# Optimization experiments

Measured on AMD Instinct MI355X. Metric: run time of the kernel, lower is better.

Reference implementation:

```python
import jax, jax.numpy as jnp
import numpy as np

N_NODES = 100000
D_SRC = 128
D_DST = 128
D_OUT = 256
N_EDGES = 600000


def setup_inputs() -> dict:
    key = jax.random.key(0)
    k1, k2, k3, k4, k5 = jax.random.split(key, 5)
    x_src = jax.random.normal(k1, (N_NODES, D_SRC), dtype=jnp.float32)
    x_dst = jax.random.normal(k2, (N_NODES, D_DST), dtype=jnp.float32)
    edge_index = jax.random.randint(k3, (2, N_EDGES), 0, N_NODES, dtype=jnp.int64)
    # Linear(in_src + in_dst, out): torch stores W as [out, in]
    fan_in = D_SRC + D_DST
    bound = 1.0 / np.sqrt(fan_in)
    W = jax.random.uniform(k4, (D_OUT, fan_in), minval=-bound, maxval=bound, dtype=jnp.float32)
    b = jax.random.uniform(k5, (D_OUT,), minval=-bound, maxval=bound, dtype=jnp.float32)
    return {"x_src": x_src, "x_dst": x_dst, "edge_index": edge_index, "W": W, "b": b}


def reference(x_src, x_dst, edge_index, W, b):
    src_idx, dst_idx = edge_index[0], edge_index[1]
    n_dst = x_dst.shape[0]
    x_j = x_src[src_idx]                                  # [E, D_SRC] gather
    summed = jax.ops.segment_sum(x_j, dst_idx, num_segments=n_dst)   # [N, D_SRC]
    count = jax.ops.segment_sum(jnp.ones((src_idx.shape[0],), dtype=x_src.dtype),
                                dst_idx, num_segments=n_dst)          # [N]
    agg = summed / jnp.maximum(count, 1.0)[:, None]        # scatter-mean
    h = jnp.concatenate([x_dst, agg], axis=-1)             # [N, D_DST+D_SRC]
    return jax.nn.relu(h @ W.T + b)                        # [N, D_OUT]
```

## Files before the change

kernel.cpp:

```cpp
#include <hip/hip_runtime.h>

#define N_NODES 100000
#define D_SRC 128
#define D_OUT 256
#define K_DIM 256
#define CAP 32
#define OVF_CAP 2048

typedef __attribute__((ext_vector_type(8))) short short8;
typedef __attribute__((ext_vector_type(4))) float float4v;

__device__ inline unsigned short f2bf(float f) {
    unsigned int u = __float_as_uint(f);
    u += 0x7FFF + ((u >> 16) & 1);
    return (unsigned short)(u >> 16);
}
__device__ inline float bf_lo(unsigned int u) { return __uint_as_float(u << 16); }
__device__ inline float bf_hi(unsigned int u) { return __uint_as_float(u & 0xFFFF0000u); }

__global__ __launch_bounds__(256) void bucket_kernel(
    const int* __restrict__ ei,
    int* __restrict__ deg,
    int* __restrict__ ovf_cnt,
    int* __restrict__ ovf,
    int* __restrict__ bucket,
    int n_edges)
{
    int e = blockIdx.x * 256 + threadIdx.x;
    if (e >= n_edges) return;
    int s = ei[e];
    int d = ei[n_edges + e];
    int pos = atomicAdd(deg + d, 1);
    if (pos < CAP) {
        bucket[(size_t)d * CAP + pos] = s;
    } else {
        int o = atomicAdd(ovf_cnt, 1);
        if (o < OVF_CAP) { ovf[2 * o] = s; ovf[2 * o + 1] = d; }
    }
}

__global__ __launch_bounds__(256) void pack_src_kernel(
    const float* __restrict__ x, unsigned short* __restrict__ xb)
{
    int i = blockIdx.x * 256 + threadIdx.x;
    float4 v = ((const float4*)x)[i];
    ushort4 o;
    o.x = f2bf(v.x); o.y = f2bf(v.y); o.z = f2bf(v.z); o.w = f2bf(v.w);
    ((ushort4*)xb)[i] = o;
}

__global__ __launch_bounds__(256) void convert_w_kernel(
    const float* __restrict__ W, unsigned short* __restrict__ Wb)
{
    int i = blockIdx.x * 256 + threadIdx.x;
    float4 v = ((const float4*)W)[i];
    ushort4 o;
    o.x = f2bf(v.x); o.y = f2bf(v.y); o.z = f2bf(v.z); o.w = f2bf(v.w);
    ((ushort4*)Wb)[i] = o;
}

__global__ __launch_bounds__(256) void gather_kernel(
    const unsigned short* __restrict__ xsb,
    const int*   __restrict__ deg,
    const int*   __restrict__ bucket,
    const int*   __restrict__ ovf_cnt,
    const int*   __restrict__ ovf,
    unsigned short* __restrict__ aggb)
{
    int node = blockIdx.x * 4 + (threadIdx.x >> 6);
    if (node >= N_NODES) return;
    int lane = threadIdx.x & 63;

    int dtot = deg[node];
    int n = (dtot < CAP) ? dtot : CAP;

    int idx = bucket[(size_t)node * CAP + (lane & 31)];

    float ax = 0.f, ay = 0.f;
    int i = 0;
    for (; i + 4 <= n; i += 4) {
        int s0 = __shfl(idx, i);
        int s1 = __shfl(idx, i + 1);
        int s2 = __shfl(idx, i + 2);
        int s3 = __shfl(idx, i + 3);
        unsigned int u0 = ((const unsigned int*)(xsb + (size_t)s0 * D_SRC))[lane];
        unsigned int u1 = ((const unsigned int*)(xsb + (size_t)s1 * D_SRC))[lane];
        unsigned int u2 = ((const unsigned int*)(xsb + (size_t)s2 * D_SRC))[lane];
        unsigned int u3 = ((const unsigned int*)(xsb + (size_t)s3 * D_SRC))[lane];
        ax += bf_lo(u0) + bf_lo(u1) + bf_lo(u2) + bf_lo(u3);
        ay += bf_hi(u0) + bf_hi(u1) + bf_hi(u2) + bf_hi(u3);
    }
    for (; i < n; ++i) {
        int s0 = __shfl(idx, i);
        unsigned int u0 = ((const unsigned int*)(xsb + (size_t)s0 * D_SRC))[lane];
        ax += bf_lo(u0);
        ay += bf_hi(u0);
    }

    if (dtot > CAP) {
        int oc = *ovf_cnt;
        if (oc > OVF_CAP) oc = OVF_CAP;
        for (int o = 0; o < oc; ++o) {
            if (ovf[2 * o + 1] == node) {
                int s0 = ovf[2 * o];
                unsigned int u0 = ((const unsigned int*)(xsb + (size_t)s0 * D_SRC))[lane];
                ax += bf_lo(u0);
                ay += bf_hi(u0);
            }
        }
    }

    float inv = 1.0f / (float)((dtot > 1) ? dtot : 1);
    unsigned int packed = (unsigned int)f2bf(ax * inv)
                        | ((unsigned int)f2bf(ay * inv) << 16);
    ((unsigned int*)(aggb + (size_t)node * D_SRC))[lane] = packed;
}

__global__ __launch_bounds__(256) void mfma_gemm_kernel(
    const float* __restrict__ x_dst,
    const unsigned short* __restrict__ aggb,
    const unsigned short* __restrict__ Wb,
    const float* __restrict__ bias,
    float*       __restrict__ out)
{
    __shared__ float eps[4][16][68];

    int wave = threadIdx.x >> 6;
    int lane = threadIdx.x & 63;
    int lrow = lane & 15;
    int kq   = lane >> 4;
    int m0 = blockIdx.x * 64;
    int n0 = wave * 64;

    float4v acc[4][4];
    #pragma unroll
    for (int i = 0; i < 4; ++i)
        #pragma unroll
        for (int j = 0; j < 4; ++j)
            acc[i][j] = (float4v){0.f, 0.f, 0.f, 0.f};

    int  rowv[4];
    bool rok[4];
    #pragma unroll
    for (int mf = 0; mf < 4; ++mf) {
        rowv[mf] = m0 + mf * 16 + lrow;
        rok[mf]  = rowv[mf] < N_NODES;
    }

    const short8 zfrag = (short8){0,0,0,0,0,0,0,0};

    #pragma unroll
    for (int kc = 0; kc < 8; ++kc) {
        const int k0 = kc * 32;
        short8 afrag[4], bfrag[4];

        if (kc < 4) {
            #pragma unroll
            for (int mf = 0; mf < 4; ++mf) {
                float4 v0 = make_float4(0.f, 0.f, 0.f, 0.f);
                float4 v1 = v0;
                if (rok[mf]) {
                    const float* p = x_dst + (size_t)rowv[mf] * D_SRC + k0 + kq * 8;
                    v0 = *(const float4*)p;
                    v1 = *(const float4*)(p + 4);
                }
                union { unsigned short s[8]; short8 v; } pk;
                pk.s[0] = f2bf(v0.x); pk.s[1] = f2bf(v0.y);
                pk.s[2] = f2bf(v0.z); pk.s[3] = f2bf(v0.w);
                pk.s[4] = f2bf(v1.x); pk.s[5] = f2bf(v1.y);
                pk.s[6] = f2bf(v1.z); pk.s[7] = f2bf(v1.w);
                afrag[mf] = pk.v;
            }
        } else {
            #pragma unroll
            for (int mf = 0; mf < 4; ++mf)
                afrag[mf] = rok[mf]
                    ? *(const short8*)(aggb + (size_t)rowv[mf] * D_SRC + (k0 - 128) + kq * 8)
                    : zfrag;
        }

        #pragma unroll
        for (int nf = 0; nf < 4; ++nf)
            bfrag[nf] = *(const short8*)(Wb + (size_t)(n0 + nf * 16 + lrow) * K_DIM + k0 + kq * 8);

        #pragma unroll
        for (int mf = 0; mf < 4; ++mf)
            #pragma unroll
            for (int nf = 0; nf < 4; ++nf)
                acc[mf][nf] = __builtin_amdgcn_mfma_f32_16x16x32_bf16(
                    afrag[mf], bfrag[nf], acc[mf][nf], 0, 0, 0);
    }

    float bv[4];
    #pragma unroll
    for (int nf = 0; nf < 4; ++nf)
        bv[nf] = bias[n0 + nf * 16 + lrow];

    int srow   = lane >> 4;
    int schunk = lane & 15;

    #pragma unroll
    for (int mf = 0; mf < 4; ++mf) {
        #pragma unroll
        for (int nf = 0; nf < 4; ++nf)
            #pragma unroll
            for (int r = 0; r < 4; ++r)
                eps[wave][kq * 4 + r][nf * 16 + lrow] =
                    fmaxf(acc[mf][nf][r] + bv[nf], 0.f);
        __syncthreads();
        #pragma unroll
        for (int c = 0; c < 4; ++c) {
            int row  = c * 4 + srow;
            float4 v = *(const float4*)&eps[wave][row][schunk * 4];
            int grow = m0 + mf * 16 + row;
            if (grow < N_NODES)
                *(float4*)(out + (size_t)grow * D_OUT + n0 + schunk * 4) = v;
        }
        __syncthreads();
    }
}

extern "C" void kernel_launch(void* const* d_in, const int* in_sizes, int n_in,
                              void* d_out, int out_size, void* d_ws, size_t ws_size,
                              hipStream_t stream) {
    const float* x_src = (const float*)d_in[0];
    const float* x_dst = (const float*)d_in[1];
    const int*   ei    = (const int*)d_in[2];
    const float* W     = (const float*)d_in[3];
    const float* bias  = (const float*)d_in[4];
    float* out = (float*)d_out;

    int n_edges = in_sizes[2] / 2;

    int* deg     = (int*)d_ws;
    int* ovf_cnt = deg + N_NODES;
    int* ovf     = ovf_cnt + 4;
    int* bucket  = ovf + OVF_CAP * 2;
    unsigned short* aggb = (unsigned short*)(bucket + (size_t)N_NODES * CAP);
    unsigned short* Wb   = aggb + (size_t)N_NODES * D_SRC;
    unsigned short* xsb  = Wb + (size_t)D_OUT * K_DIM;

    hipMemsetAsync(d_ws, 0, (N_NODES + 4) * sizeof(int), stream);

    bucket_kernel<<<(n_edges + 255) / 256, 256, 0, stream>>>(
        ei, deg, ovf_cnt, ovf, bucket, n_edges);

    pack_src_kernel<<<(N_NODES * D_SRC / 4) / 256, 256, 0, stream>>>(x_src, xsb);

    convert_w_kernel<<<(D_OUT * K_DIM / 4) / 256, 256, 0, stream>>>(W, Wb);

    gather_kernel<<<(N_NODES + 3) / 4, 256, 0, stream>>>(
        xsb, deg, bucket, ovf_cnt, ovf, aggb);

    mfma_gemm_kernel<<<(N_NODES + 63) / 64, 256, 0, stream>>>(
        x_dst, aggb, Wb, bias, out);
}
```

Before: 331.4 us.

## Pre-swizzle GEMM operands into MFMA fragment layout and double-buffer fragment loads

Adds a pre-pass that converts x_dst to bf16 and stores it in the MFMA fragment order. W and the aggregated features are also written in that order, so each lane of the GEMM does one contiguous short8 load per fragment. The GEMM now prefetches the next k-chunk's fragments into a second register set, and the per-wave epilogue uses LDS waitcnts instead of block-wide barriers. The bucket and packed-source scratch buffers move into the output buffer to free workspace. The cost is an extra full read and write pass over x_dst and higher register pressure from the double buffers.

```diff
diff --git a/kernel.cpp b/kernel.cpp
--- a/kernel.cpp
+++ b/kernel.cpp
@@ -49,14 +49,38 @@
     ((ushort4*)xb)[i] = o;
 }
 
-__global__ __launch_bounds__(256) void convert_w_kernel(
-    const float* __restrict__ W, unsigned short* __restrict__ Wb)
-{
-    int i = blockIdx.x * 256 + threadIdx.x;
-    float4 v = ((const float4*)W)[i];
-    ushort4 o;
-    o.x = f2bf(v.x); o.y = f2bf(v.y); o.z = f2bf(v.z); o.w = f2bf(v.w);
-    ((ushort4*)Wb)[i] = o;
+__global__ __launch_bounds__(256) void pack_dst_sw_kernel(
+    const float* __restrict__ x, unsigned short* __restrict__ xdsw)
+{
+    int t = blockIdx.x * 256 + threadIdx.x;
+    int r = t >> 4;
+    int g = t & 15;
+    const float4* p = (const float4*)(x + (size_t)r * 128 + g * 8);
+    float4 v0 = p[0], v1 = p[1];
+    union { unsigned short s[8]; short8 v; } pk;
+    pk.s[0] = f2bf(v0.x); pk.s[1] = f2bf(v0.y);
+    pk.s[2] = f2bf(v0.z); pk.s[3] = f2bf(v0.w);
+    pk.s[4] = f2bf(v1.x); pk.s[5] = f2bf(v1.y);
+    pk.s[6] = f2bf(v1.z); pk.s[7] = f2bf(v1.w);
+    size_t gr = ((size_t)(r >> 4) * 4 + (g >> 2)) * 64 + (r & 15) + ((g & 3) << 4);
+    ((short8*)xdsw)[gr] = pk.v;
+}
+
+__global__ __launch_bounds__(256) void convert_w_sw_kernel(
+    const float* __restrict__ W, unsigned short* __restrict__ wsw)
+{
+    int t = blockIdx.x * 256 + threadIdx.x;
+    int r = t >> 5;
+    int g = t & 31;
+    const float4* p = (const float4*)(W + (size_t)r * 256 + g * 8);
+    float4 v0 = p[0], v1 = p[1];
+    union { unsigned short s[8]; short8 v; } pk;
+    pk.s[0] = f2bf(v0.x); pk.s[1] = f2bf(v0.y);
+    pk.s[2] = f2bf(v0.z); pk.s[3] = f2bf(v0.w);
+    pk.s[4] = f2bf(v1.x); pk.s[5] = f2bf(v1.y);
+    pk.s[6] = f2bf(v1.z); pk.s[7] = f2bf(v1.w);
+    size_t gr = ((size_t)(r >> 4) * 8 + (g >> 2)) * 64 + (r & 15) + ((g & 3) << 4);
+    ((short8*)wsw)[gr] = pk.v;
 }
 
 __global__ __launch_bounds__(256) void gather_kernel(
@@ -65,7 +89,7 @@
     const int*   __restrict__ bucket,
     const int*   __restrict__ ovf_cnt,
     const int*   __restrict__ ovf,
-    unsigned short* __restrict__ aggb)
+    unsigned int* __restrict__ aggsw)
 {
     int node = blockIdx.x * 4 + (threadIdx.x >> 6);
     if (node >= N_NODES) return;
@@ -113,13 +137,15 @@
     float inv = 1.0f / (float)((dtot > 1) ? dtot : 1);
     unsigned int packed = (unsigned int)f2bf(ax * inv)
                         | ((unsigned int)f2bf(ay * inv) << 16);
-    ((unsigned int*)(aggb + (size_t)node * D_SRC))[lane] = packed;
+    size_t dw = ((size_t)(node >> 4) * 4 + (lane >> 4)) * 256
+              + (size_t)((node & 15) + 16 * ((lane >> 2) & 3)) * 4 + (lane & 3);
+    aggsw[dw] = packed;
 }
 
 __global__ __launch_bounds__(256) void mfma_gemm_kernel(
-    const float* __restrict__ x_dst,
-    const unsigned short* __restrict__ aggb,
-    const unsigned short* __restrict__ Wb,
+    const short8* __restrict__ xdsw,
+    const short8* __restrict__ aggsw,
+    const short8* __restrict__ wsw,
     const float* __restrict__ bias,
     float*       __restrict__ out)
 {
@@ -129,8 +155,17 @@
     int lane = threadIdx.x & 63;
     int lrow = lane & 15;
     int kq   = lane >> 4;
-    int m0 = blockIdx.x * 64;
-    int n0 = wave * 64;
+    int mb   = blockIdx.x;
+    int m0   = mb * 64;
+    int n0   = wave * 64;
+
+    bool mok[4];
+    #pragma unroll
+    for (int mf = 0; mf < 4; ++mf) mok[mf] = (m0 + mf * 16) < N_NODES;
+
+    const short8* Ax = xdsw  + (size_t)mb * 1024 + lane;
+    const short8* Ag = aggsw + (size_t)mb * 1024 + lane;
+    const short8* Bw = wsw   + (size_t)wave * 2048 + lane;
 
     float4v acc[4][4];
     #pragma unroll
@@ -139,56 +174,36 @@
         for (int j = 0; j < 4; ++j)
             acc[i][j] = (float4v){0.f, 0.f, 0.f, 0.f};
 
-    int  rowv[4];
-    bool rok[4];
-    #pragma unroll
-    for (int mf = 0; mf < 4; ++mf) {
-        rowv[mf] = m0 + mf * 16 + lrow;
-        rok[mf]  = rowv[mf] < N_NODES;
-    }
-
     const short8 zfrag = (short8){0,0,0,0,0,0,0,0};
+    short8 a[2][4], b[2][4];
+
+    #pragma unroll
+    for (int mf = 0; mf < 4; ++mf)
+        a[0][mf] = mok[mf] ? Ax[mf * 256] : zfrag;
+    #pragma unroll
+    for (int nf = 0; nf < 4; ++nf)
+        b[0][nf] = Bw[nf * 512];
 
     #pragma unroll
     for (int kc = 0; kc < 8; ++kc) {
-        const int k0 = kc * 32;
-        short8 afrag[4], bfrag[4];
-
-        if (kc < 4) {
-            #pragma unroll
-            for (int mf = 0; mf < 4; ++mf) {
-                float4 v0 = make_float4(0.f, 0.f, 0.f, 0.f);
-                float4 v1 = v0;
-                if (rok[mf]) {
-                    const float* p = x_dst + (size_t)rowv[mf] * D_SRC + k0 + kq * 8;
-                    v0 = *(const float4*)p;
-                    v1 = *(const float4*)(p + 4);
-                }
-                union { unsigned short s[8]; short8 v; } pk;
-                pk.s[0] = f2bf(v0.x); pk.s[1] = f2bf(v0.y);
-                pk.s[2] = f2bf(v0.z); pk.s[3] = f2bf(v0.w);
-                pk.s[4] = f2bf(v1.x); pk.s[5] = f2bf(v1.y);
-                pk.s[6] = f2bf(v1.z); pk.s[7] = f2bf(v1.w);
-                afrag[mf] = pk.v;
-            }
-        } else {
+        const int cur = kc & 1, nxt = cur ^ 1;
+        if (kc < 7) {
+            const int k1 = kc + 1;
+            const short8* A = (k1 < 4) ? Ax : Ag;
+            const int kk = (k1 < 4) ? k1 : (k1 - 4);
             #pragma unroll
             for (int mf = 0; mf < 4; ++mf)
-                afrag[mf] = rok[mf]
-                    ? *(const short8*)(aggb + (size_t)rowv[mf] * D_SRC + (k0 - 128) + kq * 8)
-                    : zfrag;
+                a[nxt][mf] = mok[mf] ? A[mf * 256 + kk * 64] : zfrag;
+            #pragma unroll
+            for (int nf = 0; nf < 4; ++nf)
+                b[nxt][nf] = Bw[nf * 512 + k1 * 64];
         }
-
-        #pragma unroll
-        for (int nf = 0; nf < 4; ++nf)
-            bfrag[nf] = *(const short8*)(Wb + (size_t)(n0 + nf * 16 + lrow) * K_DIM + k0 + kq * 8);
-
         #pragma unroll
         for (int mf = 0; mf < 4; ++mf)
             #pragma unroll
             for (int nf = 0; nf < 4; ++nf)
                 acc[mf][nf] = __builtin_amdgcn_mfma_f32_16x16x32_bf16(
-                    afrag[mf], bfrag[nf], acc[mf][nf], 0, 0, 0);
+                    a[cur][mf], b[cur][nf], acc[mf][nf], 0, 0, 0);
     }
 
     float bv[4];
@@ -201,22 +216,22 @@
 
     #pragma unroll
     for (int mf = 0; mf < 4; ++mf) {
+        if (!mok[mf]) continue;
         #pragma unroll
         for (int nf = 0; nf < 4; ++nf)
             #pragma unroll
             for (int r = 0; r < 4; ++r)
                 eps[wave][kq * 4 + r][nf * 16 + lrow] =
                     fmaxf(acc[mf][nf][r] + bv[nf], 0.f);
-        __syncthreads();
+        asm volatile("s_waitcnt lgkmcnt(0)" ::: "memory");
         #pragma unroll
         for (int c = 0; c < 4; ++c) {
             int row  = c * 4 + srow;
             float4 v = *(const float4*)&eps[wave][row][schunk * 4];
             int grow = m0 + mf * 16 + row;
-            if (grow < N_NODES)
-                *(float4*)(out + (size_t)grow * D_OUT + n0 + schunk * 4) = v;
+            *(float4*)(out + (size_t)grow * D_OUT + n0 + schunk * 4) = v;
         }
-        __syncthreads();
+        asm volatile("s_waitcnt lgkmcnt(0)" ::: "memory");
     }
 }
 
@@ -235,10 +250,12 @@
     int* deg     = (int*)d_ws;
     int* ovf_cnt = deg + N_NODES;
     int* ovf     = ovf_cnt + 4;
-    int* bucket  = ovf + OVF_CAP * 2;
-    unsigned short* aggb = (unsigned short*)(bucket + (size_t)N_NODES * CAP);
-    unsigned short* Wb   = aggb + (size_t)N_NODES * D_SRC;
-    unsigned short* xsb  = Wb + (size_t)D_OUT * K_DIM;
+    unsigned short* wsw   = (unsigned short*)(ovf + OVF_CAP * 2);
+    unsigned short* aggsw = wsw + (size_t)D_OUT * K_DIM;
+    unsigned short* xdsw  = aggsw + (size_t)(N_NODES / 16) * 4 * 64 * 8;
+
+    int* bucket = (int*)d_out;
+    unsigned short* xsb = (unsigned short*)(bucket + (size_t)N_NODES * CAP);
 
     hipMemsetAsync(d_ws, 0, (N_NODES + 4) * sizeof(int), stream);
 
@@ -247,11 +264,13 @@
 
     pack_src_kernel<<<(N_NODES * D_SRC / 4) / 256, 256, 0, stream>>>(x_src, xsb);
 
-    convert_w_kernel<<<(D_OUT * K_DIM / 4) / 256, 256, 0, stream>>>(W, Wb);
+    pack_dst_sw_kernel<<<(N_NODES * 16) / 256, 256, 0, stream>>>(x_dst, xdsw);
+
+    convert_w_sw_kernel<<<(D_OUT * K_DIM / 8) / 256, 256, 0, stream>>>(W, wsw);
 
     gather_kernel<<<(N_NODES + 3) / 4, 256, 0, stream>>>(
-        xsb, deg, bucket, ovf_cnt, ovf, aggb);
+        xsb, deg, bucket, ovf_cnt, ovf, (unsigned int*)aggsw);
 
     mfma_gemm_kernel<<<(N_NODES + 63) / 64, 256, 0, stream>>>(
-        x_dst, aggb, Wb, bias, out);
-}
+        (const short8*)xdsw, (const short8*)aggsw, (const short8*)wsw, bias, out);
+}
```

Result: faster. 314.4 us (-5.1%).
